# Optimization experiments

Hardware: AMD Instinct MI355X
Metric: run time of the kernel (lower is better)

Reference implementation:

```python
import jax, jax.numpy as jnp
import numpy as np

H = 16          # num_heads
D = 4           # att_size (hard-coded in module)
HID = 256       # hidden_size
B, N = 4, 1024
SCALE = D ** (-0.5)
BN_EPS = 1e-5
NEG_SLOPE = 0.2


def setup_inputs() -> dict:
    key = jax.random.key(0)
    ks = jax.random.split(key, 12)
    s = 0.05
    return {
        "q": jax.random.normal(ks[0], (B, HID, N), jnp.float32),
        "k": jax.random.normal(ks[1], (B, HID, N), jnp.float32),
        "v": jax.random.normal(ks[2], (B, HID, N), jnp.float32),
        "attn_bias": jax.random.normal(ks[3], (B, H, N, N), jnp.float32),
        # 1x1 Conv1d weights (kernel dim squeezed): [out_ch, in_ch]
        "Wq": jax.random.normal(ks[4], (H * D, HID), jnp.float32) * s,
        "Wk": jax.random.normal(ks[5], (H * D, HID), jnp.float32) * s,
        "Wv": jax.random.normal(ks[6], (H * D, HID), jnp.float32) * s,
        "Wo": jax.random.normal(ks[7], (HID, H * D), jnp.float32) * s,
        "bo": jax.random.normal(ks[8], (HID,), jnp.float32) * s,
        "gamma": jnp.ones((HID,), jnp.float32),
        "beta": jnp.zeros((HID,), jnp.float32),
        "run_mean": jnp.zeros((HID,), jnp.float32),
        "run_var": jnp.ones((HID,), jnp.float32),
    }


def reference(q, k, v, attn_bias, Wq, Wk, Wv, Wo, bo, gamma, beta, run_mean, run_var):
    # 1x1 conv projections: [B, HID, N] -> [B, H*D, N]
    qp = jnp.einsum('oc,bcn->bon', Wq, q)
    kp = jnp.einsum('oc,bcn->bon', Wk, k)
    vp = jnp.einsum('oc,bcn->bon', Wv, v)
    # faithful (non-standard) view: [B, H*D, N] -> [B, D, N, H]
    qh = qp.reshape(B, D, N, H).transpose(0, 3, 2, 1)   # [B, H, N, D]
    vh = vp.reshape(B, D, N, H).transpose(0, 3, 2, 1)   # [B, H, N, D]
    kh = kp.reshape(B, D, N, H).transpose(0, 3, 1, 2)   # [B, H, D, N]
    # scaled dot-product attention with additive bias
    scores = jnp.einsum('bhnd,bhdm->bhnm', qh, kh) * SCALE + attn_bias
    attn = jax.nn.softmax(scores, axis=-1)              # dropout rate 0.0 (eval)
    x = jnp.einsum('bhnm,bhmd->bhnd', attn, vh)         # [B, H, N, D]
    # transpose(3,2) then view(B, H*D, N)
    x = x.transpose(0, 1, 3, 2).reshape(B, H * D, N)
    # output 1x1 conv + BatchNorm1d (eval, running stats) + LeakyReLU(0.2)
    y = jnp.einsum('oc,bcn->bon', Wo, x) + bo[None, :, None]
    inv = jax.lax.rsqrt(run_var + BN_EPS)
    y = (y - run_mean[None, :, None]) * (gamma * inv)[None, :, None] + beta[None, :, None]
    return jnp.where(y > 0, y, NEG_SLOPE * y)
```

## Files before the change

### kernel.cpp

```cpp
#include <hip/hip_runtime.h>

#define HID 256
#define NSEQ 1024
#define NH 16
#define DH 4
#define NB 4
#define SCALEF 0.5f
#define HEADSZ (NB * NH * NSEQ * DH)

typedef float f4 __attribute__((ext_vector_type(4)));

__device__ __forceinline__ float rfl(float x) {
    return __builtin_bit_cast(float,
        __builtin_amdgcn_readfirstlane(__builtin_bit_cast(int, x)));
}

__global__ __launch_bounds__(256) void proj_kernel(
    const float* __restrict__ q, const float* __restrict__ k,
    const float* __restrict__ v, const float* __restrict__ Wq,
    const float* __restrict__ Wk, const float* __restrict__ Wv,
    float* __restrict__ ws)
{
    const int tid   = threadIdx.x;
    const int pos_l = tid & 63;
    int cb = __builtin_amdgcn_readfirstlane(tid >> 6);
    const int p    = blockIdx.y;
    const int b    = blockIdx.z;
    const int pos0 = blockIdx.x * 64;

    const float* in = (p == 0) ? q : (p == 1) ? k : v;
    const float* W  = (p == 0) ? Wq : (p == 1) ? Wk : Wv;
    float* dst = ws + (size_t)p * HEADSZ;

    __shared__ float lds_in[64][64];

    const int row_l = tid >> 4;
    const int col4  = tid & 15;
    const float* inb = in + (size_t)b * HID * NSEQ + pos0;

    float acc[16];
#pragma unroll
    for (int j = 0; j < 16; ++j) acc[j] = 0.f;

    f4 vbuf[4];
#pragma unroll
    for (int t = 0; t < 4; ++t)
        vbuf[t] = *(const f4*)(inb + (size_t)(row_l + 16 * t) * NSEQ + col4 * 4);

    for (int c = 0; c < 4; ++c) {
#pragma unroll
        for (int t = 0; t < 4; ++t)
            *(f4*)&lds_in[row_l + 16 * t][col4 * 4] = vbuf[t];
        __syncthreads();
        if (c < 3) {
#pragma unroll
            for (int t = 0; t < 4; ++t)
                vbuf[t] = *(const f4*)(inb +
                    (size_t)((c + 1) * 64 + row_l + 16 * t) * NSEQ + col4 * 4);
        }
#pragma unroll
        for (int i8 = 0; i8 < 64; i8 += 8) {
            float x[8];
#pragma unroll
            for (int j = 0; j < 8; ++j) x[j] = lds_in[i8 + j][pos_l];
#pragma unroll
            for (int kk = 0; kk < 16; ++kk) {
                const float* wr = W + (cb * 16 + kk) * HID + c * 64 + i8;
#pragma unroll
                for (int j = 0; j < 8; ++j)
                    acc[kk] = fmaf(wr[j], x[j], acc[kk]);
            }
        }
        __syncthreads();
    }

    const int pos_g = pos0 + pos_l;
    const int h     = pos_g & 15;
    const int nsub  = pos_g >> 4;
#pragma unroll
    for (int kk = 0; kk < 16; ++kk) {
        int c = cb * 16 + kk;
        int d = c >> 4;
        int n = (c & 15) * 64 + nsub;
        dst[(((size_t)b * NH + h) * NSEQ + n) * DH + d] = acc[kk];
    }
}

__global__ __launch_bounds__(256, 4) void attn_kernel(
    const float* __restrict__ bias, const float* __restrict__ ws,
    float* __restrict__ x2)
{
    const int tid  = threadIdx.x;
    const int lane = tid & 63;
    const int wave = tid >> 6;
    const int h    = blockIdx.y;
    const int b    = blockIdx.z;
    const int n0   = blockIdx.x * 32 + wave * 8;

    const float4* Qh = (const float4*)(ws);
    const float4* Kh = (const float4*)(ws + (size_t)1 * HEADSZ);
    const float4* Vh = (const float4*)(ws + (size_t)2 * HEADSZ);
    const int headbase = (b * NH + h) * NSEQ;
    const int mb = lane * 4;

    __shared__ float4 ldsK[NSEQ];
    __shared__ float4 ldsV[NSEQ];

#pragma unroll
    for (int t = 0; t < 4; ++t) {
        ldsK[tid + 256 * t] = Kh[headbase + tid + 256 * t];
        ldsV[tid + 256 * t] = Vh[headbase + tid + 256 * t];
    }

    float qx[8], qy[8], qz[8], qw[8];
#pragma unroll
    for (int r = 0; r < 8; ++r) {
        float4 t = Qh[headbase + n0 + r];
        qx[r] = rfl(t.x); qy[r] = rfl(t.y); qz[r] = rfl(t.z); qw[r] = rfl(t.w);
    }
    __syncthreads();

#define LOG2E 1.44269504f
#define EOFF  (-16.f * LOG2E)

    float sum[8];
    float o[8][4];
#pragma unroll
    for (int r = 0; r < 8; ++r) {
        sum[r] = 0.f;
        o[r][0] = o[r][1] = o[r][2] = o[r][3] = 0.f;
    }

    const float* bwave = bias + ((size_t)headbase + n0) * NSEQ + mb;

#pragma unroll 1
    for (int c = 0; c < 4; ++c) {
        float4 kb[4], vb[4];
#pragma unroll
        for (int i = 0; i < 4; ++i) {
            kb[i] = ldsK[c * 256 + mb + i];
            vb[i] = ldsV[c * 256 + mb + i];
        }
#pragma unroll
        for (int r = 0; r < 8; ++r) {
            f4 bb = __builtin_nontemporal_load(
                (const f4*)(bwave + (size_t)r * NSEQ + c * 256));
#pragma unroll
            for (int i = 0; i < 4; ++i) {
                float dot = qx[r] * kb[i].x + qy[r] * kb[i].y +
                            qz[r] * kb[i].z + qw[r] * kb[i].w;
                float s = fmaf(dot, SCALEF, bb[i]);
                float e = exp2f(fmaf(s, LOG2E, EOFF));
                sum[r] += e;
                o[r][0] = fmaf(e, vb[i].x, o[r][0]);
                o[r][1] = fmaf(e, vb[i].y, o[r][1]);
                o[r][2] = fmaf(e, vb[i].z, o[r][2]);
                o[r][3] = fmaf(e, vb[i].w, o[r][3]);
            }
        }
    }

#pragma unroll
    for (int r = 0; r < 8; ++r) {
        float s = sum[r], a0 = o[r][0], a1 = o[r][1], a2 = o[r][2], a3 = o[r][3];
#pragma unroll
        for (int st = 1; st < 64; st <<= 1) {
            s  += __shfl_xor(s,  st, 64);
            a0 += __shfl_xor(a0, st, 64);
            a1 += __shfl_xor(a1, st, 64);
            a2 += __shfl_xor(a2, st, 64);
            a3 += __shfl_xor(a3, st, 64);
        }
        float val = (lane == 0) ? a0 : (lane == 1) ? a1 : (lane == 2) ? a2 : a3;
        if (lane < 4)
            x2[((size_t)b * (NH * DH) + h * DH + lane) * NSEQ + n0 + r] = val / s;
    }
}

__global__ __launch_bounds__(256) void out_kernel(
    const float* __restrict__ x2, const float* __restrict__ Wo,
    const float* __restrict__ bo, const float* __restrict__ gamma,
    const float* __restrict__ beta, const float* __restrict__ rmean,
    const float* __restrict__ rvar, float* __restrict__ out)
{
    const int pos4 = threadIdx.x * 4;
    const int o0   = blockIdx.y * 4;
    const int b    = blockIdx.z;

    const float* xb = x2 + (size_t)b * (NH * DH) * NSEQ;

    f4 acc[4];
#pragma unroll
    for (int j = 0; j < 4; ++j) acc[j] = (f4)(0.f);

#pragma unroll 8
    for (int c = 0; c < NH * DH; ++c) {
        f4 x = *(const f4*)(xb + (size_t)c * NSEQ + pos4);
#pragma unroll
        for (int j = 0; j < 4; ++j)
            acc[j] += Wo[(o0 + j) * (NH * DH) + c] * x;
    }
#pragma unroll
    for (int j = 0; j < 4; ++j) {
        int oc = o0 + j;
        float scale = gamma[oc] * rsqrtf(rvar[oc] + 1e-5f);
        f4 y = (acc[j] + (bo[oc] - rmean[oc])) * scale + beta[oc];
        float* dst = out + ((size_t)b * HID + oc) * NSEQ + pos4;
        f4 res;
#pragma unroll
        for (int d = 0; d < 4; ++d) {
            float yy = y[d];
            res[d] = (yy > 0.f) ? yy : 0.2f * yy;
        }
        *(f4*)dst = res;
    }
}

extern "C" void kernel_launch(void* const* d_in, const int* in_sizes, int n_in,
                              void* d_out, int out_size, void* d_ws, size_t ws_size,
                              hipStream_t stream) {
    const float* q     = (const float*)d_in[0];
    const float* k     = (const float*)d_in[1];
    const float* v     = (const float*)d_in[2];
    const float* bias  = (const float*)d_in[3];
    const float* Wq    = (const float*)d_in[4];
    const float* Wk    = (const float*)d_in[5];
    const float* Wv    = (const float*)d_in[6];
    const float* Wo    = (const float*)d_in[7];
    const float* bo    = (const float*)d_in[8];
    const float* gamma = (const float*)d_in[9];
    const float* beta  = (const float*)d_in[10];
    const float* rmean = (const float*)d_in[11];
    const float* rvar  = (const float*)d_in[12];

    float* ws = (float*)d_ws;
    float* x2 = ws + (size_t)3 * HEADSZ;
    float* out = (float*)d_out;

    proj_kernel<<<dim3(NSEQ / 64, 3, NB), 256, 0, stream>>>(q, k, v, Wq, Wk, Wv, ws);
    attn_kernel<<<dim3(NSEQ / 32, NH, NB), 256, 0, stream>>>(bias, ws, x2);
    out_kernel<<<dim3(1, HID / 4, NB), 256, 0, stream>>>(
        x2, Wo, bo, gamma, beta, rmean, rvar, out);
}
```

Measured before the change: 114.6 us.

## Fuse projection, attention and output into one cooperative persistent kernel

Merges the three kernels into a single kernel launched cooperatively with 512 blocks, separated by grid-wide syncs, and falls back to three phase launches if cooperative launch fails. Each attention block now loops over four 32-row passes so K/V are staged into LDS once per 128 rows instead of once per 32, and the output stage is remapped to 1024 work units over 512 blocks. The aim is to remove launch gaps and redundant K/V loads. The cost is grid-sync overhead, only 192 of 512 blocks busy during projection, and reduced parallelism in the attention phase.

```diff
diff --git a/kernel.cpp b/kernel.cpp
--- a/kernel.cpp
+++ b/kernel.cpp
@@ -1,4 +1,5 @@
 #include <hip/hip_runtime.h>
+#include <hip/hip_cooperative_groups.h>
 
 #define HID 256
 #define NSEQ 1024
@@ -15,204 +16,212 @@
         __builtin_amdgcn_readfirstlane(__builtin_bit_cast(int, x)));
 }
 
-__global__ __launch_bounds__(256) void proj_kernel(
-    const float* __restrict__ q, const float* __restrict__ k,
-    const float* __restrict__ v, const float* __restrict__ Wq,
-    const float* __restrict__ Wk, const float* __restrict__ Wv,
-    float* __restrict__ ws)
-{
-    const int tid   = threadIdx.x;
-    const int pos_l = tid & 63;
-    int cb = __builtin_amdgcn_readfirstlane(tid >> 6);
-    const int p    = blockIdx.y;
-    const int b    = blockIdx.z;
-    const int pos0 = blockIdx.x * 64;
-
-    const float* in = (p == 0) ? q : (p == 1) ? k : v;
-    const float* W  = (p == 0) ? Wq : (p == 1) ? Wk : Wv;
-    float* dst = ws + (size_t)p * HEADSZ;
-
-    __shared__ float lds_in[64][64];
-
-    const int row_l = tid >> 4;
-    const int col4  = tid & 15;
-    const float* inb = in + (size_t)b * HID * NSEQ + pos0;
-
-    float acc[16];
-#pragma unroll
-    for (int j = 0; j < 16; ++j) acc[j] = 0.f;
-
-    f4 vbuf[4];
-#pragma unroll
-    for (int t = 0; t < 4; ++t)
-        vbuf[t] = *(const f4*)(inb + (size_t)(row_l + 16 * t) * NSEQ + col4 * 4);
-
-    for (int c = 0; c < 4; ++c) {
-#pragma unroll
-        for (int t = 0; t < 4; ++t)
-            *(f4*)&lds_in[row_l + 16 * t][col4 * 4] = vbuf[t];
-        __syncthreads();
-        if (c < 3) {
-#pragma unroll
-            for (int t = 0; t < 4; ++t)
-                vbuf[t] = *(const f4*)(inb +
-                    (size_t)((c + 1) * 64 + row_l + 16 * t) * NSEQ + col4 * 4);
-        }
-#pragma unroll
-        for (int i8 = 0; i8 < 64; i8 += 8) {
-            float x[8];
-#pragma unroll
-            for (int j = 0; j < 8; ++j) x[j] = lds_in[i8 + j][pos_l];
-#pragma unroll
-            for (int kk = 0; kk < 16; ++kk) {
-                const float* wr = W + (cb * 16 + kk) * HID + c * 64 + i8;
-#pragma unroll
-                for (int j = 0; j < 8; ++j)
-                    acc[kk] = fmaf(wr[j], x[j], acc[kk]);
-            }
-        }
-        __syncthreads();
-    }
-
-    const int pos_g = pos0 + pos_l;
-    const int h     = pos_g & 15;
-    const int nsub  = pos_g >> 4;
-#pragma unroll
-    for (int kk = 0; kk < 16; ++kk) {
-        int c = cb * 16 + kk;
-        int d = c >> 4;
-        int n = (c & 15) * 64 + nsub;
-        dst[(((size_t)b * NH + h) * NSEQ + n) * DH + d] = acc[kk];
-    }
-}
-
-__global__ __launch_bounds__(256, 4) void attn_kernel(
-    const float* __restrict__ bias, const float* __restrict__ ws,
-    float* __restrict__ x2)
-{
-    const int tid  = threadIdx.x;
-    const int lane = tid & 63;
-    const int wave = tid >> 6;
-    const int h    = blockIdx.y;
-    const int b    = blockIdx.z;
-    const int n0   = blockIdx.x * 32 + wave * 8;
-
-    const float4* Qh = (const float4*)(ws);
-    const float4* Kh = (const float4*)(ws + (size_t)1 * HEADSZ);
-    const float4* Vh = (const float4*)(ws + (size_t)2 * HEADSZ);
-    const int headbase = (b * NH + h) * NSEQ;
-    const int mb = lane * 4;
-
-    __shared__ float4 ldsK[NSEQ];
-    __shared__ float4 ldsV[NSEQ];
-
-#pragma unroll
-    for (int t = 0; t < 4; ++t) {
-        ldsK[tid + 256 * t] = Kh[headbase + tid + 256 * t];
-        ldsV[tid + 256 * t] = Vh[headbase + tid + 256 * t];
-    }
-
-    float qx[8], qy[8], qz[8], qw[8];
-#pragma unroll
-    for (int r = 0; r < 8; ++r) {
-        float4 t = Qh[headbase + n0 + r];
-        qx[r] = rfl(t.x); qy[r] = rfl(t.y); qz[r] = rfl(t.z); qw[r] = rfl(t.w);
-    }
-    __syncthreads();
-
 #define LOG2E 1.44269504f
 #define EOFF  (-16.f * LOG2E)
 
-    float sum[8];
-    float o[8][4];
-#pragma unroll
-    for (int r = 0; r < 8; ++r) {
-        sum[r] = 0.f;
-        o[r][0] = o[r][1] = o[r][2] = o[r][3] = 0.f;
-    }
-
-    const float* bwave = bias + ((size_t)headbase + n0) * NSEQ + mb;
-
-#pragma unroll 1
-    for (int c = 0; c < 4; ++c) {
-        float4 kb[4], vb[4];
-#pragma unroll
-        for (int i = 0; i < 4; ++i) {
-            kb[i] = ldsK[c * 256 + mb + i];
-            vb[i] = ldsV[c * 256 + mb + i];
-        }
-#pragma unroll
-        for (int r = 0; r < 8; ++r) {
-            f4 bb = __builtin_nontemporal_load(
-                (const f4*)(bwave + (size_t)r * NSEQ + c * 256));
-#pragma unroll
-            for (int i = 0; i < 4; ++i) {
-                float dot = qx[r] * kb[i].x + qy[r] * kb[i].y +
-                            qz[r] * kb[i].z + qw[r] * kb[i].w;
-                float s = fmaf(dot, SCALEF, bb[i]);
-                float e = exp2f(fmaf(s, LOG2E, EOFF));
-                sum[r] += e;
-                o[r][0] = fmaf(e, vb[i].x, o[r][0]);
-                o[r][1] = fmaf(e, vb[i].y, o[r][1]);
-                o[r][2] = fmaf(e, vb[i].z, o[r][2]);
-                o[r][3] = fmaf(e, vb[i].w, o[r][3]);
-            }
-        }
-    }
-
-#pragma unroll
-    for (int r = 0; r < 8; ++r) {
-        float s = sum[r], a0 = o[r][0], a1 = o[r][1], a2 = o[r][2], a3 = o[r][3];
-#pragma unroll
-        for (int st = 1; st < 64; st <<= 1) {
-            s  += __shfl_xor(s,  st, 64);
-            a0 += __shfl_xor(a0, st, 64);
-            a1 += __shfl_xor(a1, st, 64);
-            a2 += __shfl_xor(a2, st, 64);
-            a3 += __shfl_xor(a3, st, 64);
-        }
-        float val = (lane == 0) ? a0 : (lane == 1) ? a1 : (lane == 2) ? a2 : a3;
-        if (lane < 4)
-            x2[((size_t)b * (NH * DH) + h * DH + lane) * NSEQ + n0 + r] = val / s;
-    }
-}
-
-__global__ __launch_bounds__(256) void out_kernel(
-    const float* __restrict__ x2, const float* __restrict__ Wo,
+__global__ __launch_bounds__(256, 4) void fused_kernel(
+    const float* __restrict__ q, const float* __restrict__ k,
+    const float* __restrict__ v, const float* __restrict__ bias,
+    const float* __restrict__ Wq, const float* __restrict__ Wk,
+    const float* __restrict__ Wv, const float* __restrict__ Wo,
     const float* __restrict__ bo, const float* __restrict__ gamma,
     const float* __restrict__ beta, const float* __restrict__ rmean,
-    const float* __restrict__ rvar, float* __restrict__ out)
+    const float* __restrict__ rvar, float* ws, float* out, int phase)
 {
-    const int pos4 = threadIdx.x * 4;
-    const int o0   = blockIdx.y * 4;
-    const int b    = blockIdx.z;
-
-    const float* xb = x2 + (size_t)b * (NH * DH) * NSEQ;
-
-    f4 acc[4];
-#pragma unroll
-    for (int j = 0; j < 4; ++j) acc[j] = (f4)(0.f);
-
-#pragma unroll 8
-    for (int c = 0; c < NH * DH; ++c) {
-        f4 x = *(const f4*)(xb + (size_t)c * NSEQ + pos4);
-#pragma unroll
-        for (int j = 0; j < 4; ++j)
-            acc[j] += Wo[(o0 + j) * (NH * DH) + c] * x;
-    }
-#pragma unroll
-    for (int j = 0; j < 4; ++j) {
-        int oc = o0 + j;
-        float scale = gamma[oc] * rsqrtf(rvar[oc] + 1e-5f);
-        f4 y = (acc[j] + (bo[oc] - rmean[oc])) * scale + beta[oc];
-        float* dst = out + ((size_t)b * HID + oc) * NSEQ + pos4;
-        f4 res;
-#pragma unroll
-        for (int d = 0; d < 4; ++d) {
-            float yy = y[d];
-            res[d] = (yy > 0.f) ? yy : 0.2f * yy;
-        }
-        *(f4*)dst = res;
+    __shared__ float smem[8192];
+    const int tid  = threadIdx.x;
+    const int blk  = blockIdx.x;
+    const bool coop = (phase < 0);
+    float* x2 = ws + (size_t)3 * HEADSZ;
+
+    if ((coop || phase == 0) && blk < 192) {
+        const int pos0 = (blk & 15) * 64;
+        const int p    = (blk >> 4) % 3;
+        const int b    = blk / 48;
+        const float* in = (p == 0) ? q : (p == 1) ? k : v;
+        const float* W  = (p == 0) ? Wq : (p == 1) ? Wk : Wv;
+        float* dst = ws + (size_t)p * HEADSZ;
+
+        float (*lds_in)[64] = (float(*)[64])smem;
+        const int pos_l = tid & 63;
+        int cb = __builtin_amdgcn_readfirstlane(tid >> 6);
+        const int row_l = tid >> 4;
+        const int col4  = tid & 15;
+        const float* inb = in + (size_t)b * HID * NSEQ + pos0;
+
+        float acc[16];
+#pragma unroll
+        for (int j = 0; j < 16; ++j) acc[j] = 0.f;
+
+        f4 vbuf[4];
+#pragma unroll
+        for (int t = 0; t < 4; ++t)
+            vbuf[t] = *(const f4*)(inb + (size_t)(row_l + 16 * t) * NSEQ + col4 * 4);
+
+        for (int c = 0; c < 4; ++c) {
+#pragma unroll
+            for (int t = 0; t < 4; ++t)
+                *(f4*)&lds_in[row_l + 16 * t][col4 * 4] = vbuf[t];
+            __syncthreads();
+            if (c < 3) {
+#pragma unroll
+                for (int t = 0; t < 4; ++t)
+                    vbuf[t] = *(const f4*)(inb +
+                        (size_t)((c + 1) * 64 + row_l + 16 * t) * NSEQ + col4 * 4);
+            }
+#pragma unroll
+            for (int i8 = 0; i8 < 64; i8 += 8) {
+                float x[8];
+#pragma unroll
+                for (int j = 0; j < 8; ++j) x[j] = lds_in[i8 + j][pos_l];
+#pragma unroll
+                for (int kk = 0; kk < 16; ++kk) {
+                    const float* wr = W + (cb * 16 + kk) * HID + c * 64 + i8;
+#pragma unroll
+                    for (int j = 0; j < 8; ++j)
+                        acc[kk] = fmaf(wr[j], x[j], acc[kk]);
+                }
+            }
+            __syncthreads();
+        }
+
+        const int pos_g = pos0 + pos_l;
+        const int hh    = pos_g & 15;
+        const int nsub  = pos_g >> 4;
+#pragma unroll
+        for (int kk = 0; kk < 16; ++kk) {
+            int c = cb * 16 + kk;
+            int d = c >> 4;
+            int n = (c & 15) * 64 + nsub;
+            dst[(((size_t)b * NH + hh) * NSEQ + n) * DH + d] = acc[kk];
+        }
+    }
+
+    if (coop) cooperative_groups::this_grid().sync();
+
+    if (coop || phase == 1) {
+        const int b    = blk >> 7;
+        const int h    = (blk >> 3) & 15;
+        const int seg  = blk & 7;
+        const int lane = tid & 63;
+        const int wave = tid >> 6;
+
+        const float4* Qh = (const float4*)(ws);
+        const float4* Kh = (const float4*)(ws + (size_t)1 * HEADSZ);
+        const float4* Vh = (const float4*)(ws + (size_t)2 * HEADSZ);
+        const int headbase = (b * NH + h) * NSEQ;
+        const int mb = lane * 4;
+
+        float4* ldsK = (float4*)smem;
+        float4* ldsV = ldsK + NSEQ;
+
+        __syncthreads();
+#pragma unroll
+        for (int t = 0; t < 4; ++t) {
+            ldsK[tid + 256 * t] = Kh[headbase + tid + 256 * t];
+            ldsV[tid + 256 * t] = Vh[headbase + tid + 256 * t];
+        }
+        __syncthreads();
+
+#pragma unroll 1
+        for (int pass = 0; pass < 4; ++pass) {
+            const int n0 = seg * 128 + pass * 32 + wave * 8;
+
+            float qx[8], qy[8], qz[8], qw[8];
+#pragma unroll
+            for (int r = 0; r < 8; ++r) {
+                float4 t = Qh[headbase + n0 + r];
+                qx[r] = rfl(t.x); qy[r] = rfl(t.y);
+                qz[r] = rfl(t.z); qw[r] = rfl(t.w);
+            }
+
+            float sum[8];
+            float o[8][4];
+#pragma unroll
+            for (int r = 0; r < 8; ++r) {
+                sum[r] = 0.f;
+                o[r][0] = o[r][1] = o[r][2] = o[r][3] = 0.f;
+            }
+
+            const float* bwave = bias + ((size_t)headbase + n0) * NSEQ + mb;
+
+#pragma unroll 1
+            for (int c = 0; c < 4; ++c) {
+                float4 kb[4], vb[4];
+#pragma unroll
+                for (int i = 0; i < 4; ++i) {
+                    kb[i] = ldsK[c * 256 + mb + i];
+                    vb[i] = ldsV[c * 256 + mb + i];
+                }
+#pragma unroll
+                for (int r = 0; r < 8; ++r) {
+                    f4 bb = __builtin_nontemporal_load(
+                        (const f4*)(bwave + (size_t)r * NSEQ + c * 256));
+#pragma unroll
+                    for (int i = 0; i < 4; ++i) {
+                        float dot = qx[r] * kb[i].x + qy[r] * kb[i].y +
+                                    qz[r] * kb[i].z + qw[r] * kb[i].w;
+                        float s = fmaf(dot, SCALEF, bb[i]);
+                        float e = exp2f(fmaf(s, LOG2E, EOFF));
+                        sum[r] += e;
+                        o[r][0] = fmaf(e, vb[i].x, o[r][0]);
+                        o[r][1] = fmaf(e, vb[i].y, o[r][1]);
+                        o[r][2] = fmaf(e, vb[i].z, o[r][2]);
+                        o[r][3] = fmaf(e, vb[i].w, o[r][3]);
+                    }
+                }
+            }
+
+#pragma unroll
+            for (int r = 0; r < 8; ++r) {
+                float s = sum[r], a0 = o[r][0], a1 = o[r][1],
+                      a2 = o[r][2], a3 = o[r][3];
+#pragma unroll
+                for (int st = 1; st < 64; st <<= 1) {
+                    s  += __shfl_xor(s,  st, 64);
+                    a0 += __shfl_xor(a0, st, 64);
+                    a1 += __shfl_xor(a1, st, 64);
+                    a2 += __shfl_xor(a2, st, 64);
+                    a3 += __shfl_xor(a3, st, 64);
+                }
+                float val = (lane == 0) ? a0 : (lane == 1) ? a1
+                          : (lane == 2) ? a2 : a3;
+                if (lane < 4)
+                    x2[((size_t)b * (NH * DH) + h * DH + lane) * NSEQ + n0 + r] =
+                        val / s;
+            }
+        }
+    }
+
+    if (coop) cooperative_groups::this_grid().sync();
+
+    if (coop || phase == 2) {
+#pragma unroll 1
+        for (int u = blk; u < 1024; u += 512) {
+            const int b      = u >> 8;
+            const int r      = u & 255;
+            const int chquad = r >> 2;
+            const int posq   = r & 3;
+            const int oc     = chquad * 4 + (tid >> 6);
+            const int pos    = posq * 256 + (tid & 63) * 4;
+
+            const float* xb = x2 + (size_t)b * (NH * DH) * NSEQ;
+            f4 acc = (f4)(0.f);
+#pragma unroll 16
+            for (int c = 0; c < NH * DH; ++c) {
+                f4 x = *(const f4*)(xb + (size_t)c * NSEQ + pos);
+                acc += Wo[oc * (NH * DH) + c] * x;
+            }
+            float scale = gamma[oc] * rsqrtf(rvar[oc] + 1e-5f);
+            f4 y = (acc + (bo[oc] - rmean[oc])) * scale + beta[oc];
+            f4 res;
+#pragma unroll
+            for (int d = 0; d < 4; ++d) {
+                float yy = y[d];
+                res[d] = (yy > 0.f) ? yy : 0.2f * yy;
+            }
+            *(f4*)(out + ((size_t)b * HID + oc) * NSEQ + pos) = res;
+        }
     }
 }
 
@@ -233,12 +242,28 @@
     const float* rmean = (const float*)d_in[11];
     const float* rvar  = (const float*)d_in[12];
 
-    float* ws = (float*)d_ws;
-    float* x2 = ws + (size_t)3 * HEADSZ;
+    float* ws  = (float*)d_ws;
     float* out = (float*)d_out;
-
-    proj_kernel<<<dim3(NSEQ / 64, 3, NB), 256, 0, stream>>>(q, k, v, Wq, Wk, Wv, ws);
-    attn_kernel<<<dim3(NSEQ / 32, NH, NB), 256, 0, stream>>>(bias, ws, x2);
-    out_kernel<<<dim3(1, HID / 4, NB), 256, 0, stream>>>(
-        x2, Wo, bo, gamma, beta, rmean, rvar, out);
+    int phase = -1;
+
+    void* args[] = {
+        (void*)&q, (void*)&k, (void*)&v, (void*)&bias,
+        (void*)&Wq, (void*)&Wk, (void*)&Wv, (void*)&Wo,
+        (void*)&bo, (void*)&gamma, (void*)&beta, (void*)&rmean,
+        (void*)&rvar, (void*)&ws, (void*)&out, (void*)&phase
+    };
+    hipError_t e = hipLaunchCooperativeKernel((void*)fused_kernel, dim3(512),
+                                              dim3(256), args, 0, stream);
+    if (e != hipSuccess) {
+        (void)hipGetLastError();
+        fused_kernel<<<dim3(512), dim3(256), 0, stream>>>(
+            q, k, v, bias, Wq, Wk, Wv, Wo, bo, gamma, beta, rmean, rvar,
+            ws, out, 0);
+        fused_kernel<<<dim3(512), dim3(256), 0, stream>>>(
+            q, k, v, bias, Wq, Wk, Wv, Wo, bo, gamma, beta, rmean, rvar,
+            ws, out, 1);
+        fused_kernel<<<dim3(512), dim3(256), 0, stream>>>(
+            q, k, v, bias, Wq, Wk, Wv, Wo, bo, gamma, beta, rmean, rvar,
+            ws, out, 2);
+    }
 }
```

After: 250.5 us. 2.19x slower.
